# Kernel optimization log

Measured on AMD Instinct MI355X. Metric: run time of the kernel, lower is better.

## Reference

```python
import jax, jax.numpy as jnp
import numpy as np

# SLAYER neuron / simulation parameters (from network.yaml)
THETA = 10.0      # spike threshold
TAU_SR = 10.0     # SRM (psp) kernel time constant
TAU_REF = 1.0     # refractory kernel time constant
SCALE_REF = 2.0   # refractory scale (kernel = -scaleRef*theta*alpha(t))
TS = 1.0          # simulation step (ms)
TK = 100          # FIR truncation length for the psp kernel (tauSr=10 -> fully decayed)

B, NIN, NHID, NOUT, T = 32, 2312, 512, 10, 350

# discrete refractory kernel ref[n] = C_REF * n * D_REF**n  (alpha shape)
D_REF = float(np.exp(-TS / TAU_REF))
C_REF = float(-SCALE_REF * THETA * np.e * TS / TAU_REF)


def srm_kernel():
    # eps(t) = (t/tauSr) * exp(1 - t/tauSr), peak value 1 at t = tauSr
    t = jnp.arange(TK, dtype=jnp.float32) * TS
    return (t / TAU_SR) * jnp.exp(1.0 - t / TAU_SR)


def psp(x):
    """Causal FIR filter along time. x: [B, C, T] -> [B, C, T]."""
    b, c, t = x.shape
    k = srm_kernel()[::-1].reshape(1, 1, TK)  # lax.conv correlates, so flip
    xp = jnp.pad(x.reshape(b * c, 1, t), ((0, 0), (0, 0), (TK - 1, 0)))
    y = jax.lax.conv_general_dilated(xp, k, (1,), 'VALID')
    return y.reshape(b, c, t)


def dense(W, x):
    # 1x1 conv over channels, applied at every time step
    return jnp.einsum('oi,bit->bot', W, x)


@jax.custom_vjp
def spike_fn(u):
    return (u >= THETA).astype(u.dtype)

def _spike_fwd(u):
    return spike_fn(u), u

def _spike_bwd(u, g):
    # SLAYER surrogate gradient: rho(u) = scaleRho * exp(-|u - theta| / tauRho)
    return (g * jnp.exp(-jnp.abs(u - THETA) / 1.0),)

spike_fn.defvjp(_spike_fwd, _spike_bwd)


def spike_layer(u_in):
    """Threshold-and-refractory spike dynamics via a 2-state IIR realization of
    the alpha refractory kernel. u_in: [B, C, T] -> spikes [B, C, T]."""
    uT = jnp.moveaxis(u_in, -1, 0)  # [T, B, C]
    zero = jnp.zeros(uT.shape[1:], uT.dtype)

    def step(carry, u_t):
        a, b = carry  # a = conv(spikes, D^n), b = conv(spikes, n*D^n)
        u = u_t + C_REF * b          # membrane = psp drive + refractory
        s = spike_fn(u)
        a_new = D_REF * a + s
        b_new = D_REF * b + D_REF * a
        return (a_new, b_new), s

    _, sT = jax.lax.scan(step, (zero, zero), uT)
    return jnp.moveaxis(sT, 0, -1)


def setup_inputs() -> dict:
    key = jax.random.key(0)
    k1, k2, k3 = jax.random.split(key, 3)
    spikeInput = (jax.random.uniform(k1, (B, NIN, T)) < 0.05).astype(jnp.float32)
    W1 = jax.random.normal(k2, (NHID, NIN), dtype=jnp.float32) * 0.05
    W2 = jax.random.normal(k3, (NOUT, NHID), dtype=jnp.float32) * 0.05
    return {"spikeInput": spikeInput, "W1": W1, "W2": W2}


def reference(spikeInput, W1, W2):
    s1 = spike_layer(dense(W1, psp(spikeInput)))
    s2 = spike_layer(dense(W2, psp(s1)))
    return s2
```

## Files before the change

kernel.cpp:

```cpp
#include <hip/hip_runtime.h>
#include <stdint.h>

#define B_SZ   32
#define NIN    2312
#define NHID   512
#define NOUT   10
#define T_SZ   350
#define NW32   73
#define NW64   8
#define NHALF  256
#define NROW   2313

#define DS_D   0.9048374180359595
#define CS_D   0.2718281828459045
#define D100_D 4.5399929762484854e-05
#define DREF_F 0.36787944117144233f
#define CREF_F -54.36563656918091f

#define NCHUNK 7
#define CLEN   50
#define NPF    10

__global__ __launch_bounds__(384) void k12(const float* __restrict__ x,
                                           const float* __restrict__ W1,
                                           uint32_t* __restrict__ bits1,
                                           float* __restrict__ W1s) {
    __shared__ float lds[32 * T_SZ];
    const int bid = blockIdx.x;
    const int tid = threadIdx.x;
    if (bid < NW32 * B_SZ) {
        const int w = bid % NW32;
        const int b = bid / NW32;
        const int rows = (NIN - (w << 5) < 32) ? (NIN - (w << 5)) : 32;
        const float* base = x + ((size_t)(b * NIN + (w << 5))) * T_SZ;
        const int nf2 = rows * (T_SZ / 2);
        for (int f = tid; f < nf2; f += 384)
            ((float2*)lds)[f] = ((const float2*)base)[f];
        __syncthreads();
        if (tid < T_SZ) {
            uint32_t bits = 0;
            for (int j = 0; j < rows; ++j)
                bits |= (lds[j * T_SZ + tid] > 0.5f) ? (1u << j) : 0u;
            bits1[(size_t)(b * T_SZ + tid) * NW32 + w] = bits;
        }
    } else if (bid < NW32 * B_SZ + NW32 * 16) {
        float (*tile)[33] = (float (*)[33])lds;
        const int bb = bid - NW32 * B_SZ;
        const int i0 = (bb % NW32) * 32, o0 = (bb / NW32) * 32;
        const int tx = tid & 31, ty = tid >> 5;
#pragma unroll
        for (int r = 0; r < 3; ++r) {
            int row = ty + 12 * r;
            if (row < 32) {
                int o = o0 + row, i = i0 + tx;
                if (i < NIN) tile[row][tx] = W1[(size_t)o * NIN + i];
            }
        }
        __syncthreads();
#pragma unroll
        for (int r = 0; r < 3; ++r) {
            int row = ty + 12 * r;
            if (row < 32) {
                int i = i0 + row, o = o0 + tx;
                if (i < NIN)
                    W1s[((size_t)(o >> 8) * NROW + i) * NHALF + (o & 255)] = tile[tx][row];
            }
        }
    } else {
        if (tid < NHALF) {
            W1s[((size_t)0 * NROW + NIN) * NHALF + tid] = 0.0f;
            W1s[((size_t)1 * NROW + NIN) * NHALF + tid] = 0.0f;
        }
    }
}

__global__ __launch_bounds__(256) void k3_dense1(const uint32_t* __restrict__ bits1,
                                                 const float* __restrict__ W1s,
                                                 float* __restrict__ z1ct) {
    __shared__ uint32_t words[128];
    __shared__ uint16_t pfx[80];
    __shared__ uint16_t idxbuf[NIN + 16];
    __shared__ float red[3][NHALF];
    __shared__ float fin[NHALF];

    const int bt = blockIdx.x;
    const int h = blockIdx.y;
    const int tid = threadIdx.x;
    const int wv = tid >> 6, lane = tid & 63;

    if (tid < 128) words[tid] = (tid < NW32) ? bits1[(size_t)bt * NW32 + tid] : 0u;
    __syncthreads();

    if (wv == 0) {
        uint32_t w0 = words[lane];
        uint32_t w1 = words[lane + 64];
        int p0 = __popc(w0), p1 = __popc(w1);
        int s0 = p0, s1 = p1;
#pragma unroll
        for (int off = 1; off < 64; off <<= 1) {
            int u0 = __shfl_up(s0, off);
            int u1 = __shfl_up(s1, off);
            if (lane >= off) { s0 += u0; s1 += u1; }
        }
        int tot0 = __shfl(s0, 63);
        pfx[lane] = (uint16_t)(s0 - p0);
        if (lane < 9) pfx[lane + 64] = (uint16_t)(tot0 + s1 - p1);
        if (lane == 8) pfx[73] = (uint16_t)(tot0 + s1);
    }
    __syncthreads();

    const int ntot = pfx[73];
    const int npad = (ntot + 15) & ~15;
    if (tid < NW32) {
        uint32_t m = words[tid];
        int p = pfx[tid];
        while (m) {
            int j = __builtin_ctz(m);
            m &= m - 1;
            idxbuf[p++] = (uint16_t)((tid << 5) + j);
        }
    }
    if (tid >= 240) {
        int k = tid - 240;
        if (ntot + k < npad) idxbuf[ntot + k] = (uint16_t)NIN;
    }
    __syncthreads();

    const float* Wh = W1s + (size_t)h * NROW * NHALF;
    float4 acc = make_float4(0.f, 0.f, 0.f, 0.f);
    for (int r = wv; r < npad; r += 16) {
        int i0 = idxbuf[r], i1 = idxbuf[r + 4], i2 = idxbuf[r + 8], i3 = idxbuf[r + 12];
        float4 v0 = ((const float4*)(Wh + (size_t)i0 * NHALF))[lane];
        float4 v1 = ((const float4*)(Wh + (size_t)i1 * NHALF))[lane];
        float4 v2 = ((const float4*)(Wh + (size_t)i2 * NHALF))[lane];
        float4 v3 = ((const float4*)(Wh + (size_t)i3 * NHALF))[lane];
        acc.x += v0.x; acc.y += v0.y; acc.z += v0.z; acc.w += v0.w;
        acc.x += v1.x; acc.y += v1.y; acc.z += v1.z; acc.w += v1.w;
        acc.x += v2.x; acc.y += v2.y; acc.z += v2.z; acc.w += v2.w;
        acc.x += v3.x; acc.y += v3.y; acc.z += v3.z; acc.w += v3.w;
    }
    if (wv > 0) ((float4*)red[wv - 1])[lane] = acc;
    __syncthreads();
    if (wv == 0) {
        float4 a1 = ((float4*)red[0])[lane];
        float4 a2 = ((float4*)red[1])[lane];
        float4 a3 = ((float4*)red[2])[lane];
        acc.x = ((acc.x + a1.x) + a2.x) + a3.x;
        acc.y = ((acc.y + a1.y) + a2.y) + a3.y;
        acc.z = ((acc.z + a1.z) + a2.z) + a3.z;
        acc.w = ((acc.w + a1.w) + a2.w) + a3.w;
        ((float4*)fin)[lane] = acc;
    }
    __syncthreads();
    const int och = (h << 8) + tid;
    const int oc = och >> 6, l6 = och & 63;
    const int b = bt / T_SZ, t = bt - b * T_SZ;
    z1ct[((size_t)(b * NW64 + oc) * T_SZ + t) * 64 + l6] = fin[tid];
}

__global__ __launch_bounds__(64) void k4_fir_scan1(const float* __restrict__ z1ct,
                                                   uint64_t* __restrict__ s1bits) {
    const int lane = threadIdx.x;
    const int bc = blockIdx.x / NCHUNK;
    const int ck = blockIdx.x % NCHUNK;
    const int tstart = ck * CLEN;
    const int tend = tstart + CLEN;
    const int t0 = (tstart >= 100) ? tstart - 100 : 0;
    const float* base = z1ct + (size_t)bc * T_SZ * 64 + lane;
    uint64_t* outp = s1bits + (size_t)bc * T_SZ;
    double A = 0.0, Bs = 0.0, A2 = 0.0, Bs2 = 0.0;
    float ra = 0.0f, rb = 0.0f;
    const double TAIL = D100_D * CS_D;
    float xb[NPF], xdb[NPF];
#pragma unroll
    for (int i = 0; i < NPF; ++i) {
        int t = t0 + i;
        xb[i] = base[(size_t)t * 64];
        int td = t - 100;
        xdb[i] = (td >= 0) ? base[(size_t)td * 64] : 0.0f;
    }
    for (int tb = t0; tb < tend; tb += NPF) {
#pragma unroll
        for (int i = 0; i < NPF; ++i) {
            const int t = tb + i;
            float x = xb[i], xd = xdb[i];
            const int tn = t + NPF;
            xb[i] = (tn < T_SZ) ? base[(size_t)tn * 64] : 0.0f;
            const int td = tn - 100;
            xdb[i] = (td >= 0) ? base[(size_t)td * 64] : 0.0f;
            Bs = DS_D * Bs + DS_D * A;
            A = DS_D * A + (double)x;
            Bs2 = DS_D * Bs2 + DS_D * A2;
            A2 = DS_D * A2 + (double)xd;
            double y = CS_D * Bs - TAIL * (Bs2 + 100.0 * A2);
            float u = (float)y + CREF_F * rb;
            float s = (u >= 10.0f) ? 1.0f : 0.0f;
            float ran = DREF_F * ra + s;
            float rbn = DREF_F * rb + DREF_F * ra;
            ra = ran; rb = rbn;
            uint64_t mball = __ballot(s != 0.0f);
            if (t >= tstart && lane == 0) outp[t] = mball;
        }
    }
}

__global__ __launch_bounds__(256) void k5_dense2(const uint64_t* __restrict__ s1bits,
                                                 const float* __restrict__ W2,
                                                 float* __restrict__ z2ct) {
    __shared__ float W2s[NHID * NOUT];
    for (int k = threadIdx.x; k < NHID * NOUT; k += 256) {
        int c = k / NOUT, o = k - c * NOUT;
        W2s[k] = W2[(size_t)o * NHID + c];
    }
    __syncthreads();
    int idx = blockIdx.x * 256 + threadIdx.x;
    if (idx >= T_SZ * B_SZ * NOUT) return;
    int t = idx / (B_SZ * NOUT);
    int bo = idx - t * (B_SZ * NOUT);
    int b = bo / NOUT;
    int o = bo - b * NOUT;
    float acc = 0.f;
    const uint64_t* bp = s1bits + (size_t)b * NW64 * T_SZ + t;
#pragma unroll
    for (int wv = 0; wv < NW64; ++wv) {
        uint64_t m = bp[(size_t)wv * T_SZ];
        while (m) {
            int j = __builtin_ctzll(m);
            m &= m - 1;
            acc += W2s[((wv << 6) + j) * NOUT + o];
        }
    }
    z2ct[((size_t)(bo >> 6) * T_SZ + t) * 64 + (bo & 63)] = acc;
}

__global__ __launch_bounds__(64) void k6_fir_scan2(const float* __restrict__ z2ct,
                                                   float* __restrict__ out) {
    const int lane = threadIdx.x;
    const int g = blockIdx.x / NCHUNK;
    const int ck = blockIdx.x % NCHUNK;
    const int tstart = ck * CLEN;
    const int tend = tstart + CLEN;
    const int t0 = (tstart >= 100) ? tstart - 100 : 0;
    const int bo = (g << 6) + lane;
    const float* base = z2ct + (size_t)g * T_SZ * 64 + lane;
    float* op = out + (size_t)bo * T_SZ;
    double A = 0.0, Bs = 0.0, A2 = 0.0, Bs2 = 0.0;
    float ra = 0.0f, rb = 0.0f;
    const double TAIL = D100_D * CS_D;
    float xb[NPF], xdb[NPF];
#pragma unroll
    for (int i = 0; i < NPF; ++i) {
        int t = t0 + i;
        xb[i] = base[(size_t)t * 64];
        int td = t - 100;
        xdb[i] = (td >= 0) ? base[(size_t)td * 64] : 0.0f;
    }
    for (int tb = t0; tb < tend; tb += NPF) {
#pragma unroll
        for (int i = 0; i < NPF; ++i) {
            const int t = tb + i;
            float x = xb[i], xd = xdb[i];
            const int tn = t + NPF;
            xb[i] = (tn < T_SZ) ? base[(size_t)tn * 64] : 0.0f;
            const int td = tn - 100;
            xdb[i] = (td >= 0) ? base[(size_t)td * 64] : 0.0f;
            Bs = DS_D * Bs + DS_D * A;
            A = DS_D * A + (double)x;
            Bs2 = DS_D * Bs2 + DS_D * A2;
            A2 = DS_D * A2 + (double)xd;
            double y = CS_D * Bs - TAIL * (Bs2 + 100.0 * A2);
            float u = (float)y + CREF_F * rb;
            float s = (u >= 10.0f) ? 1.0f : 0.0f;
            float ran = DREF_F * ra + s;
            float rbn = DREF_F * rb + DREF_F * ra;
            ra = ran; rb = rbn;
            if (t >= tstart) op[t] = s;
        }
    }
}

extern "C" void kernel_launch(void* const* d_in, const int* in_sizes, int n_in,
                              void* d_out, int out_size, void* d_ws, size_t ws_size,
                              hipStream_t stream) {
    const float* spikeInput = (const float*)d_in[0];
    const float* W1 = (const float*)d_in[1];
    const float* W2 = (const float*)d_in[2];
    float* out = (float*)d_out;

    char* ws = (char*)d_ws;
    float* W1s = (float*)(ws + 0);
    uint32_t* bits1 = (uint32_t*)(ws + 4737024);
    float* z1ct = (float*)(ws + 8007424);
    uint64_t* s1bits = (uint64_t*)(ws + 30945024);
    float* z2ct = (float*)(ws + 4737024);

    k12<<<NW32 * B_SZ + NW32 * 16 + 1, 384, 0, stream>>>(spikeInput, W1, bits1, W1s);
    k3_dense1<<<dim3(B_SZ * T_SZ, 2), 256, 0, stream>>>(bits1, W1s, z1ct);
    k4_fir_scan1<<<B_SZ * NW64 * NCHUNK, 64, 0, stream>>>(z1ct, s1bits);
    k5_dense2<<<(T_SZ * B_SZ * NOUT + 255) / 256, 256, 0, stream>>>(s1bits, W2, z2ct);
    k6_fir_scan2<<<5 * NCHUNK, 64, 0, stream>>>(z2ct, out);
}
```

Baseline: 333.8 us.

## Make dense1 weight-stationary: stream W1 slices through LDS, reuse across 44 columns

The first dense layer is rewritten so each of 256 blocks owns 44 (batch,time) columns. All of transposed W1 is streamed through LDS in 32-row slices, double-buffered through registers, and each column's spike bitmask selects which LDS rows to accumulate. Before, every (b,t) block gathered its active W1 rows from global memory separately. The change reuses each loaded weight slice across many columns, cutting L2/HBM traffic, and drops the prefix-sum/index compaction. The cost is one block per CU with about 140KB of LDS, low occupancy and serial per-bit LDS reads.

```diff
diff --git a/kernel.cpp b/kernel.cpp
--- a/kernel.cpp
+++ b/kernel.cpp
@@ -8,8 +8,7 @@
 #define T_SZ   350
 #define NW32   73
 #define NW64   8
-#define NHALF  256
-#define NROW   2313
+#define NROWP  2336
 
 #define DS_D   0.9048374180359595
 #define CS_D   0.2718281828459045
@@ -21,10 +20,15 @@
 #define CLEN   50
 #define NPF    10
 
+#define C_PB   44
+#define NBLK3  256
+#define SROWS  32
+#define NSLICE 73
+
 __global__ __launch_bounds__(384) void k12(const float* __restrict__ x,
                                            const float* __restrict__ W1,
                                            uint32_t* __restrict__ bits1,
-                                           float* __restrict__ W1s) {
+                                           float* __restrict__ W1t) {
     __shared__ float lds[32 * T_SZ];
     const int bid = blockIdx.x;
     const int tid = threadIdx.x;
@@ -43,7 +47,7 @@
                 bits |= (lds[j * T_SZ + tid] > 0.5f) ? (1u << j) : 0u;
             bits1[(size_t)(b * T_SZ + tid) * NW32 + w] = bits;
         }
-    } else if (bid < NW32 * B_SZ + NW32 * 16) {
+    } else {
         float (*tile)[33] = (float (*)[33])lds;
         const int bb = bid - NW32 * B_SZ;
         const int i0 = (bb % NW32) * 32, o0 = (bb / NW32) * 32;
@@ -62,100 +66,76 @@
             int row = ty + 12 * r;
             if (row < 32) {
                 int i = i0 + row, o = o0 + tx;
-                if (i < NIN)
-                    W1s[((size_t)(o >> 8) * NROW + i) * NHALF + (o & 255)] = tile[tx][row];
+                if (i < NIN) W1t[(size_t)i * NHID + o] = tile[tx][row];
             }
         }
-    } else {
-        if (tid < NHALF) {
-            W1s[((size_t)0 * NROW + NIN) * NHALF + tid] = 0.0f;
-            W1s[((size_t)1 * NROW + NIN) * NHALF + tid] = 0.0f;
-        }
-    }
-}
-
-__global__ __launch_bounds__(256) void k3_dense1(const uint32_t* __restrict__ bits1,
-                                                 const float* __restrict__ W1s,
-                                                 float* __restrict__ z1ct) {
-    __shared__ uint32_t words[128];
-    __shared__ uint16_t pfx[80];
-    __shared__ uint16_t idxbuf[NIN + 16];
-    __shared__ float red[3][NHALF];
-    __shared__ float fin[NHALF];
-
-    const int bt = blockIdx.x;
-    const int h = blockIdx.y;
+    }
+}
+
+__global__ __launch_bounds__(256, 1) void k3_dense1(const uint32_t* __restrict__ bits1,
+                                                    const float* __restrict__ W1t,
+                                                    float* __restrict__ z1ct) {
+    __shared__ float sbuf[2][SROWS * NHID];
+    __shared__ uint32_t cb[C_PB][NSLICE];
     const int tid = threadIdx.x;
-    const int wv = tid >> 6, lane = tid & 63;
-
-    if (tid < 128) words[tid] = (tid < NW32) ? bits1[(size_t)bt * NW32 + tid] : 0u;
+    const int c0 = blockIdx.x * C_PB;
+
+    for (int k = tid; k < C_PB * NSLICE; k += 256) {
+        int c = k / NSLICE, w = k - c * NSLICE;
+        int cg = c0 + c;
+        cb[c][w] = (cg < B_SZ * T_SZ) ? bits1[(size_t)cg * NW32 + w] : 0u;
+    }
+
+    const float4* G = (const float4*)W1t;
+    float4 stg[16];
+#pragma unroll
+    for (int k = 0; k < 16; ++k) stg[k] = G[k * 256 + tid];
+
+    float2 acc[C_PB];
+#pragma unroll
+    for (int c = 0; c < C_PB; ++c) acc[c] = make_float2(0.f, 0.f);
+
+#pragma unroll
+    for (int k = 0; k < 16; ++k) ((float4*)sbuf[0])[k * 256 + tid] = stg[k];
     __syncthreads();
 
-    if (wv == 0) {
-        uint32_t w0 = words[lane];
-        uint32_t w1 = words[lane + 64];
-        int p0 = __popc(w0), p1 = __popc(w1);
-        int s0 = p0, s1 = p1;
-#pragma unroll
-        for (int off = 1; off < 64; off <<= 1) {
-            int u0 = __shfl_up(s0, off);
-            int u1 = __shfl_up(s1, off);
-            if (lane >= off) { s0 += u0; s1 += u1; }
-        }
-        int tot0 = __shfl(s0, 63);
-        pfx[lane] = (uint16_t)(s0 - p0);
-        if (lane < 9) pfx[lane + 64] = (uint16_t)(tot0 + s1 - p1);
-        if (lane == 8) pfx[73] = (uint16_t)(tot0 + s1);
-    }
-    __syncthreads();
-
-    const int ntot = pfx[73];
-    const int npad = (ntot + 15) & ~15;
-    if (tid < NW32) {
-        uint32_t m = words[tid];
-        int p = pfx[tid];
-        while (m) {
-            int j = __builtin_ctz(m);
-            m &= m - 1;
-            idxbuf[p++] = (uint16_t)((tid << 5) + j);
-        }
-    }
-    if (tid >= 240) {
-        int k = tid - 240;
-        if (ntot + k < npad) idxbuf[ntot + k] = (uint16_t)NIN;
-    }
-    __syncthreads();
-
-    const float* Wh = W1s + (size_t)h * NROW * NHALF;
-    float4 acc = make_float4(0.f, 0.f, 0.f, 0.f);
-    for (int r = wv; r < npad; r += 16) {
-        int i0 = idxbuf[r], i1 = idxbuf[r + 4], i2 = idxbuf[r + 8], i3 = idxbuf[r + 12];
-        float4 v0 = ((const float4*)(Wh + (size_t)i0 * NHALF))[lane];
-        float4 v1 = ((const float4*)(Wh + (size_t)i1 * NHALF))[lane];
-        float4 v2 = ((const float4*)(Wh + (size_t)i2 * NHALF))[lane];
-        float4 v3 = ((const float4*)(Wh + (size_t)i3 * NHALF))[lane];
-        acc.x += v0.x; acc.y += v0.y; acc.z += v0.z; acc.w += v0.w;
-        acc.x += v1.x; acc.y += v1.y; acc.z += v1.z; acc.w += v1.w;
-        acc.x += v2.x; acc.y += v2.y; acc.z += v2.z; acc.w += v2.w;
-        acc.x += v3.x; acc.y += v3.y; acc.z += v3.z; acc.w += v3.w;
-    }
-    if (wv > 0) ((float4*)red[wv - 1])[lane] = acc;
-    __syncthreads();
-    if (wv == 0) {
-        float4 a1 = ((float4*)red[0])[lane];
-        float4 a2 = ((float4*)red[1])[lane];
-        float4 a3 = ((float4*)red[2])[lane];
-        acc.x = ((acc.x + a1.x) + a2.x) + a3.x;
-        acc.y = ((acc.y + a1.y) + a2.y) + a3.y;
-        acc.z = ((acc.z + a1.z) + a2.z) + a3.z;
-        acc.w = ((acc.w + a1.w) + a2.w) + a3.w;
-        ((float4*)fin)[lane] = acc;
-    }
-    __syncthreads();
-    const int och = (h << 8) + tid;
-    const int oc = och >> 6, l6 = och & 63;
-    const int b = bt / T_SZ, t = bt - b * T_SZ;
-    z1ct[((size_t)(b * NW64 + oc) * T_SZ + t) * 64 + l6] = fin[tid];
+    for (int s = 0; s < NSLICE; ++s) {
+        const int p = s & 1;
+        if (s + 1 < NSLICE) {
+#pragma unroll
+            for (int k = 0; k < 16; ++k)
+                stg[k] = G[(size_t)(s + 1) * 4096 + k * 256 + tid];
+        }
+        const float2* sp = (const float2*)sbuf[p];
+#pragma unroll
+        for (int c = 0; c < C_PB; ++c) {
+            uint32_t m = cb[c][s];
+            while (m) {
+                int j = __builtin_ctz(m);
+                m &= m - 1;
+                float2 v = sp[j * 256 + tid];
+                acc[c].x += v.x;
+                acc[c].y += v.y;
+            }
+        }
+        if (s + 1 < NSLICE) {
+#pragma unroll
+            for (int k = 0; k < 16; ++k)
+                ((float4*)sbuf[p ^ 1])[k * 256 + tid] = stg[k];
+        }
+        __syncthreads();
+    }
+
+    const int o = tid * 2;
+    const int oc = o >> 6, l6 = o & 63;
+#pragma unroll
+    for (int c = 0; c < C_PB; ++c) {
+        int cg = c0 + c;
+        if (cg < B_SZ * T_SZ) {
+            int b = cg / T_SZ, t = cg - b * T_SZ;
+            *(float2*)(z1ct + ((size_t)(b * NW64 + oc) * T_SZ + t) * 64 + l6) = acc[c];
+        }
+    }
 }
 
 __global__ __launch_bounds__(64) void k4_fir_scan1(const float* __restrict__ z1ct,
@@ -288,14 +268,14 @@
     float* out = (float*)d_out;
 
     char* ws = (char*)d_ws;
-    float* W1s = (float*)(ws + 0);
-    uint32_t* bits1 = (uint32_t*)(ws + 4737024);
-    float* z1ct = (float*)(ws + 8007424);
-    uint64_t* s1bits = (uint64_t*)(ws + 30945024);
-    float* z2ct = (float*)(ws + 4737024);
-
-    k12<<<NW32 * B_SZ + NW32 * 16 + 1, 384, 0, stream>>>(spikeInput, W1, bits1, W1s);
-    k3_dense1<<<dim3(B_SZ * T_SZ, 2), 256, 0, stream>>>(bits1, W1s, z1ct);
+    float* W1t = (float*)(ws + 0);
+    uint32_t* bits1 = (uint32_t*)(ws + 4784128);
+    float* z1ct = (float*)(ws + 8054528);
+    uint64_t* s1bits = (uint64_t*)(ws + 30992128);
+    float* z2ct = (float*)(ws + 4784128);
+
+    k12<<<NW32 * B_SZ + NW32 * 16, 384, 0, stream>>>(spikeInput, W1, bits1, W1t);
+    k3_dense1<<<NBLK3, 256, 0, stream>>>(bits1, W1t, z1ct);
     k4_fir_scan1<<<B_SZ * NW64 * NCHUNK, 64, 0, stream>>>(z1ct, s1bits);
     k5_dense2<<<(T_SZ * B_SZ * NOUT + 255) / 256, 256, 0, stream>>>(s1bits, W2, z2ct);
     k6_fir_scan2<<<5 * NCHUNK, 64, 0, stream>>>(z2ct, out);
```

Result: slower. 857.8 us (+156.9%).

## Fuse hidden-layer FIR/spike scan with second dense layer; widen input loads

Applied to the files above, without the earlier changes.

Merges the layer-1 FIR/refractory scan and the sparse layer-2 dense into one kernel. Each block covers one batch and one time chunk across all 8 channel-waves, keeps the spike bitmasks in LDS, and accumulates W2 directly. This drops one launch and the global round trip of the spike bitmasks. The input bit-pack loader also moves from float2 to float4 loads. In exchange, the scan grid shrinks from 1792 blocks of 64 threads to 224 blocks of 512, and each block reloads W2 into LDS, which may lower parallelism.

```diff
diff --git a/kernel.cpp b/kernel.cpp
--- a/kernel.cpp
+++ b/kernel.cpp
@@ -33,9 +33,9 @@
         const int b = bid / NW32;
         const int rows = (NIN - (w << 5) < 32) ? (NIN - (w << 5)) : 32;
         const float* base = x + ((size_t)(b * NIN + (w << 5))) * T_SZ;
-        const int nf2 = rows * (T_SZ / 2);
-        for (int f = tid; f < nf2; f += 384)
-            ((float2*)lds)[f] = ((const float2*)base)[f];
+        const int nf4 = (rows * T_SZ) >> 2;
+        for (int f = tid; f < nf4; f += 384)
+            ((float4*)lds)[f] = ((const float4*)base)[f];
         __syncthreads();
         if (tid < T_SZ) {
             uint32_t bits = 0;
@@ -158,16 +158,25 @@
     z1ct[((size_t)(b * NW64 + oc) * T_SZ + t) * 64 + l6] = fin[tid];
 }
 
-__global__ __launch_bounds__(64) void k4_fir_scan1(const float* __restrict__ z1ct,
-                                                   uint64_t* __restrict__ s1bits) {
-    const int lane = threadIdx.x;
-    const int bc = blockIdx.x / NCHUNK;
+__global__ __launch_bounds__(512) void k45(const float* __restrict__ z1ct,
+                                           const float* __restrict__ W2,
+                                           float* __restrict__ z2ct) {
+    __shared__ float W2s[NHID * NOUT];
+    __shared__ uint64_t sw[CLEN][NW64];
+    const int tid = threadIdx.x;
+    const int wv = tid >> 6, lane = tid & 63;
+    const int b = blockIdx.x / NCHUNK;
     const int ck = blockIdx.x % NCHUNK;
     const int tstart = ck * CLEN;
     const int tend = tstart + CLEN;
     const int t0 = (tstart >= 100) ? tstart - 100 : 0;
-    const float* base = z1ct + (size_t)bc * T_SZ * 64 + lane;
-    uint64_t* outp = s1bits + (size_t)bc * T_SZ;
+
+    for (int k = tid; k < NHID * NOUT; k += 512) {
+        int c = k / NOUT, o = k - c * NOUT;
+        W2s[k] = W2[(size_t)o * NHID + c];
+    }
+
+    const float* base = z1ct + (size_t)(b * NW64 + wv) * T_SZ * 64 + lane;
     double A = 0.0, Bs = 0.0, A2 = 0.0, Bs2 = 0.0;
     float ra = 0.0f, rb = 0.0f;
     const double TAIL = D100_D * CS_D;
@@ -199,38 +208,28 @@
             float rbn = DREF_F * rb + DREF_F * ra;
             ra = ran; rb = rbn;
             uint64_t mball = __ballot(s != 0.0f);
-            if (t >= tstart && lane == 0) outp[t] = mball;
-        }
-    }
-}
-
-__global__ __launch_bounds__(256) void k5_dense2(const uint64_t* __restrict__ s1bits,
-                                                 const float* __restrict__ W2,
-                                                 float* __restrict__ z2ct) {
-    __shared__ float W2s[NHID * NOUT];
-    for (int k = threadIdx.x; k < NHID * NOUT; k += 256) {
-        int c = k / NOUT, o = k - c * NOUT;
-        W2s[k] = W2[(size_t)o * NHID + c];
-    }
-    __syncthreads();
-    int idx = blockIdx.x * 256 + threadIdx.x;
-    if (idx >= T_SZ * B_SZ * NOUT) return;
-    int t = idx / (B_SZ * NOUT);
-    int bo = idx - t * (B_SZ * NOUT);
-    int b = bo / NOUT;
-    int o = bo - b * NOUT;
-    float acc = 0.f;
-    const uint64_t* bp = s1bits + (size_t)b * NW64 * T_SZ + t;
-#pragma unroll
-    for (int wv = 0; wv < NW64; ++wv) {
-        uint64_t m = bp[(size_t)wv * T_SZ];
-        while (m) {
-            int j = __builtin_ctzll(m);
-            m &= m - 1;
-            acc += W2s[((wv << 6) + j) * NOUT + o];
-        }
-    }
-    z2ct[((size_t)(bo >> 6) * T_SZ + t) * 64 + (bo & 63)] = acc;
+            if (t >= tstart && lane == 0) sw[t - tstart][wv] = mball;
+        }
+    }
+    __syncthreads();
+
+    if (tid < CLEN * NOUT) {
+        const int tr = tid / NOUT;
+        const int o = tid - tr * NOUT;
+        const int t = tstart + tr;
+        float acc = 0.f;
+#pragma unroll
+        for (int w2 = 0; w2 < NW64; ++w2) {
+            uint64_t m = sw[tr][w2];
+            while (m) {
+                int j = __builtin_ctzll(m);
+                m &= m - 1;
+                acc += W2s[((w2 << 6) + j) * NOUT + o];
+            }
+        }
+        const int bo = b * NOUT + o;
+        z2ct[((size_t)(bo >> 6) * T_SZ + t) * 64 + (bo & 63)] = acc;
+    }
 }
 
 __global__ __launch_bounds__(64) void k6_fir_scan2(const float* __restrict__ z2ct,
@@ -291,12 +290,10 @@
     float* W1s = (float*)(ws + 0);
     uint32_t* bits1 = (uint32_t*)(ws + 4737024);
     float* z1ct = (float*)(ws + 8007424);
-    uint64_t* s1bits = (uint64_t*)(ws + 30945024);
     float* z2ct = (float*)(ws + 4737024);
 
     k12<<<NW32 * B_SZ + NW32 * 16 + 1, 384, 0, stream>>>(spikeInput, W1, bits1, W1s);
     k3_dense1<<<dim3(B_SZ * T_SZ, 2), 256, 0, stream>>>(bits1, W1s, z1ct);
-    k4_fir_scan1<<<B_SZ * NW64 * NCHUNK, 64, 0, stream>>>(z1ct, s1bits);
-    k5_dense2<<<(T_SZ * B_SZ * NOUT + 255) / 256, 256, 0, stream>>>(s1bits, W2, z2ct);
+    k45<<<B_SZ * NCHUNK, 512, 0, stream>>>(z1ct, W2, z2ct);
     k6_fir_scan2<<<5 * NCHUNK, 64, 0, stream>>>(z2ct, out);
 }
```

Measured after the change: 316.4 us (median of 2 runs). 1.06x faster.
